# Optimization experiments

Hardware: AMD Instinct MI355X
Metric: run time of the kernel (lower is better)

The kernel has to match this reference:

```python
import jax, jax.numpy as jnp
import numpy as np

SIZE = 256  # matrix dimension n; input vector length = n*(n-1)/2
BATCH = 512

# strictly-lower indices in the same row-major (i, j<i) order as the module's l_indices
_ROWS, _COLS = np.tril_indices(SIZE, k=-1)


def setup_inputs() -> dict:
    key = jax.random.key(0)
    m = SIZE * (SIZE - 1) // 2
    # z entries are partial-correlation-like values, must lie in (-1, 1)
    vec = jax.random.uniform(key, (BATCH, m), dtype=jnp.float32, minval=-0.99, maxval=0.99)
    return {"vec": vec}


def reference(vec):
    B = vec.shape[0]
    n = SIZE
    # scatter vector into strictly-lower triangle: (B, n, n)
    z = jnp.zeros((B, n, n), dtype=vec.dtype).at[:, _ROWS, _COLS].set(vec)
    signs = jnp.sign(z)
    signs = jnp.where(signs == 0, jnp.asarray(1.0, vec.dtype), signs)
    z2 = z * z

    row_idx = jnp.arange(n)  # (n,)

    def step(rowsum, inp):
        # rowsum: (B, n) running sum of x_squared over already-built columns, per row
        j, z2_col = inp  # z2_col: (B, n) = z^2[:, :, j]
        base = z2_col * (1.0 - rowsum)           # lower entries (rows > j)
        col = jnp.where(row_idx[None, :] == j, jnp.asarray(1.0, vec.dtype),
                        jnp.where(row_idx[None, :] < j, jnp.asarray(0.0, vec.dtype), base))
        return rowsum + col, col

    z2_cols = jnp.moveaxis(z2, -1, 0)  # (n_col, B, n_row)
    _, x2_cols = jax.lax.scan(step, jnp.zeros((B, n), dtype=vec.dtype),
                              (jnp.arange(n), z2_cols))
    # x2_cols: (n_col, B, n_row) -> (B, n_row, n_col)
    x2 = jnp.moveaxis(x2_cols, 0, -1)
    return jnp.sqrt(x2) * signs
```

## Files before the change

kernel.cpp:

```cpp
#include <hip/hip_runtime.h>


#define SIZE 256
#define BATCH 512
#define M (SIZE * (SIZE - 1) / 2)
#define TOTAL (BATCH * M)

typedef float f4u __attribute__((ext_vector_type(4), aligned(4)));

template <int CTRL, int ROW_MASK>
__device__ __forceinline__ float scan_mul(float p) {
    int sh = __builtin_amdgcn_update_dpp(
        __builtin_bit_cast(int, 1.0f),
        __builtin_bit_cast(int, p),
        CTRL, ROW_MASK, 0xF, false);
    return p * __builtin_bit_cast(float, sh);
}

__device__ __forceinline__ float excl_shift_one(float p) {
    int r = __builtin_amdgcn_update_dpp(
        __builtin_bit_cast(int, 1.0f),
        __builtin_bit_cast(int, p),
        0x138 , 0xF, 0xF, false);
    return __builtin_bit_cast(float, r);
}

__global__ __launch_bounds__(256) void chol_from_z_kernel(
    const float* __restrict__ vec, float* __restrict__ out) {
    const int lane = threadIdx.x & 63;
    const int wib = __builtin_amdgcn_readfirstlane((int)threadIdx.x >> 6);
    const int wave = (int)blockIdx.x * 4 + wib;
    const int b = wave >> 8;
    const int i = wave & 255;
    const int row_off = b * M + ((i * (i - 1)) >> 1);
    const float* __restrict__ s = vec + row_off;
    float* __restrict__ dst = out + ((size_t)wave << 8);
    const int j0 = lane << 2;

    const int maxidx = (TOTAL - 1) - row_off;
    f4u zv;
    if (j0 + 3 <= maxidx) {
        zv = *(const f4u*)(s + j0);
    } else {
        zv.x = s[j0]; zv.y = s[j0 + 1]; zv.z = s[j0 + 2]; zv.w = 0.f;
    }

    const float z0 = (j0     < i) ? zv.x : 0.f;
    const float z1 = (j0 + 1 < i) ? zv.y : 0.f;
    const float z2 = (j0 + 2 < i) ? zv.z : 0.f;
    const float z3 = (j0 + 3 < i) ? zv.w : 0.f;

    const float t0 = 1.f - z0 * z0;
    const float t1 = 1.f - z1 * z1;
    const float t2 = 1.f - z2 * z2;
    const float t3 = 1.f - z3 * z3;

    float p = (t0 * t1) * (t2 * t3);

    p = scan_mul<0x111, 0xF>(p);
    p = scan_mul<0x112, 0xF>(p);
    p = scan_mul<0x114, 0xF>(p);
    p = scan_mul<0x118, 0xF>(p);
    if (i >= 64)  p = scan_mul<0x142, 0xA>(p);
    if (i >= 128) p = scan_mul<0x143, 0xC>(p);

    float run = excl_shift_one(p);

    f4u o;
    o.x = (j0     == i) ? 1.f : z0 * __builtin_amdgcn_sqrtf(run); run *= t0;
    o.y = (j0 + 1 == i) ? 1.f : z1 * __builtin_amdgcn_sqrtf(run); run *= t1;
    o.z = (j0 + 2 == i) ? 1.f : z2 * __builtin_amdgcn_sqrtf(run); run *= t2;
    o.w = (j0 + 3 == i) ? 1.f : z3 * __builtin_amdgcn_sqrtf(run);

    *(f4u*)(dst + j0) = o;
}

extern "C" void kernel_launch(void* const* d_in, const int* in_sizes, int n_in,
                              void* d_out, int out_size, void* d_ws, size_t ws_size,
                              hipStream_t stream) {
    const float* vec = (const float*)d_in[0];
    float* out = (float*)d_out;
    const int n_waves = BATCH * SIZE;
    const int blocks = n_waves / 4;
    chol_from_z_kernel<<<blocks, 256, 0, stream>>>(vec, out);
}
```

Measured before the change: 175.3 us.

## Process two rows per wave with XCD block swizzle and nontemporal stores

Each wave now computes two adjacent output rows, interleaving their loads, DPP prefix-product scans and sqrt chains to expose more independent memory and ALU work. Block indices are remapped so that consecutive blocks dispatched to the same XCD cover contiguous data. Output stores become 16-byte aligned nontemporal stores to avoid polluting cache with write-only data. This halves the wave count and raises per-thread register use, which may reduce occupancy.

```diff
diff --git a/kernel.cpp b/kernel.cpp
--- a/kernel.cpp
+++ b/kernel.cpp
@@ -5,8 +5,11 @@
 #define BATCH 512
 #define M (SIZE * (SIZE - 1) / 2)
 #define TOTAL (BATCH * M)
+#define NWAVES (BATCH * SIZE / 2)
+#define NBLOCKS (NWAVES / 4)
 
 typedef float f4u __attribute__((ext_vector_type(4), aligned(4)));
+typedef float f4a __attribute__((ext_vector_type(4), aligned(16)));
 
 template <int CTRL, int ROW_MASK>
 __device__ __forceinline__ float scan_mul(float p) {
@@ -29,50 +32,73 @@
     const float* __restrict__ vec, float* __restrict__ out) {
     const int lane = threadIdx.x & 63;
     const int wib = __builtin_amdgcn_readfirstlane((int)threadIdx.x >> 6);
-    const int wave = (int)blockIdx.x * 4 + wib;
-    const int b = wave >> 8;
-    const int i = wave & 255;
-    const int row_off = b * M + ((i * (i - 1)) >> 1);
-    const float* __restrict__ s = vec + row_off;
-    float* __restrict__ dst = out + ((size_t)wave << 8);
+
+    const int bid = (int)blockIdx.x;
+    const int sbid = (bid & 7) * (NBLOCKS / 8) + (bid >> 3);
+
+    const int wave = sbid * 4 + wib;
+    const int r0 = wave << 1;
+    const int b = r0 >> 8;
+    const int i0 = r0 & 255;
+    const int i1 = i0 + 1;
+    const int off0 = b * M + ((i0 * (i0 - 1)) >> 1);
+    const int off1 = off0 + i0;
+    const float* __restrict__ sA = vec + off0;
+    const float* __restrict__ sB = vec + off1;
+    float* __restrict__ dst = out + ((size_t)r0 << 8);
     const int j0 = lane << 2;
 
-    const int maxidx = (TOTAL - 1) - row_off;
-    f4u zv;
-    if (j0 + 3 <= maxidx) {
-        zv = *(const f4u*)(s + j0);
+    f4u za = *(const f4u*)(sA + j0);
+    f4u zb;
+    if (off1 + 255 < TOTAL) {
+        zb = *(const f4u*)(sB + j0);
     } else {
-        zv.x = s[j0]; zv.y = s[j0 + 1]; zv.z = s[j0 + 2]; zv.w = 0.f;
+        const int maxidx = (TOTAL - 1) - off1;
+        zb.x = sB[j0]; zb.y = sB[j0 + 1]; zb.z = sB[j0 + 2];
+        zb.w = (j0 + 3 <= maxidx) ? sB[j0 + 3] : 0.f;
     }
 
-    const float z0 = (j0     < i) ? zv.x : 0.f;
-    const float z1 = (j0 + 1 < i) ? zv.y : 0.f;
-    const float z2 = (j0 + 2 < i) ? zv.z : 0.f;
-    const float z3 = (j0 + 3 < i) ? zv.w : 0.f;
+    const float a0 = (j0     < i0) ? za.x : 0.f;
+    const float a1 = (j0 + 1 < i0) ? za.y : 0.f;
+    const float a2 = (j0 + 2 < i0) ? za.z : 0.f;
+    const float a3 = (j0 + 3 < i0) ? za.w : 0.f;
+    const float b0 = (j0     < i1) ? zb.x : 0.f;
+    const float b1 = (j0 + 1 < i1) ? zb.y : 0.f;
+    const float b2 = (j0 + 2 < i1) ? zb.z : 0.f;
+    const float b3 = (j0 + 3 < i1) ? zb.w : 0.f;
 
-    const float t0 = 1.f - z0 * z0;
-    const float t1 = 1.f - z1 * z1;
-    const float t2 = 1.f - z2 * z2;
-    const float t3 = 1.f - z3 * z3;
+    const float tA0 = 1.f - a0 * a0, tA1 = 1.f - a1 * a1;
+    const float tA2 = 1.f - a2 * a2, tA3 = 1.f - a3 * a3;
+    const float tB0 = 1.f - b0 * b0, tB1 = 1.f - b1 * b1;
+    const float tB2 = 1.f - b2 * b2, tB3 = 1.f - b3 * b3;
 
-    float p = (t0 * t1) * (t2 * t3);
+    float pA = (tA0 * tA1) * (tA2 * tA3);
+    float pB = (tB0 * tB1) * (tB2 * tB3);
 
-    p = scan_mul<0x111, 0xF>(p);
-    p = scan_mul<0x112, 0xF>(p);
-    p = scan_mul<0x114, 0xF>(p);
-    p = scan_mul<0x118, 0xF>(p);
-    if (i >= 64)  p = scan_mul<0x142, 0xA>(p);
-    if (i >= 128) p = scan_mul<0x143, 0xC>(p);
+    pA = scan_mul<0x111, 0xF>(pA);  pB = scan_mul<0x111, 0xF>(pB);
+    pA = scan_mul<0x112, 0xF>(pA);  pB = scan_mul<0x112, 0xF>(pB);
+    pA = scan_mul<0x114, 0xF>(pA);  pB = scan_mul<0x114, 0xF>(pB);
+    pA = scan_mul<0x118, 0xF>(pA);  pB = scan_mul<0x118, 0xF>(pB);
+    if (i0 >= 64)  { pA = scan_mul<0x142, 0xA>(pA);
+                     pB = scan_mul<0x142, 0xA>(pB); }
+    if (i0 >= 128) { pA = scan_mul<0x143, 0xC>(pA);
+                     pB = scan_mul<0x143, 0xC>(pB); }
 
-    float run = excl_shift_one(p);
+    float runA = excl_shift_one(pA);
+    float runB = excl_shift_one(pB);
 
-    f4u o;
-    o.x = (j0     == i) ? 1.f : z0 * __builtin_amdgcn_sqrtf(run); run *= t0;
-    o.y = (j0 + 1 == i) ? 1.f : z1 * __builtin_amdgcn_sqrtf(run); run *= t1;
-    o.z = (j0 + 2 == i) ? 1.f : z2 * __builtin_amdgcn_sqrtf(run); run *= t2;
-    o.w = (j0 + 3 == i) ? 1.f : z3 * __builtin_amdgcn_sqrtf(run);
+    f4a oA, oB;
+    oA.x = (j0     == i0) ? 1.f : a0 * __builtin_amdgcn_sqrtf(runA); runA *= tA0;
+    oB.x = (j0     == i1) ? 1.f : b0 * __builtin_amdgcn_sqrtf(runB); runB *= tB0;
+    oA.y = (j0 + 1 == i0) ? 1.f : a1 * __builtin_amdgcn_sqrtf(runA); runA *= tA1;
+    oB.y = (j0 + 1 == i1) ? 1.f : b1 * __builtin_amdgcn_sqrtf(runB); runB *= tB1;
+    oA.z = (j0 + 2 == i0) ? 1.f : a2 * __builtin_amdgcn_sqrtf(runA); runA *= tA2;
+    oB.z = (j0 + 2 == i1) ? 1.f : b2 * __builtin_amdgcn_sqrtf(runB); runB *= tB2;
+    oA.w = (j0 + 3 == i0) ? 1.f : a3 * __builtin_amdgcn_sqrtf(runA);
+    oB.w = (j0 + 3 == i1) ? 1.f : b3 * __builtin_amdgcn_sqrtf(runB);
 
-    *(f4u*)(dst + j0) = o;
+    __builtin_nontemporal_store(oA, (f4a*)(dst + j0));
+    __builtin_nontemporal_store(oB, (f4a*)(dst + SIZE + j0));
 }
 
 extern "C" void kernel_launch(void* const* d_in, const int* in_sizes, int n_in,
@@ -80,7 +106,5 @@
                               hipStream_t stream) {
     const float* vec = (const float*)d_in[0];
     float* out = (float*)d_out;
-    const int n_waves = BATCH * SIZE;
-    const int blocks = n_waves / 4;
-    chol_from_z_kernel<<<blocks, 256, 0, stream>>>(vec, out);
+    chol_from_z_kernel<<<NBLOCKS, 256, 0, stream>>>(vec, out);
 }
```

New measurement: 182.5 us. 4.1% more time.
